# Kernel tuning notes

Hardware: AMD Instinct MI355X
Metric: run time of the kernel (lower is better)

Reference implementation:

```python
import jax, jax.numpy as jnp
import numpy as np

B, L, IN_DIM, H, KD = 2, 2048, 1024, 16, 64
SCALE = float(np.sqrt(IN_DIM / H))  # sqrt(in_dim / num_heads), per ScaledDotAttention
LN_EPS = 1e-5


def setup_inputs() -> dict:
    key = jax.random.key(0)
    ks = jax.random.split(key, 12)
    s_in = 1.0 / np.sqrt(IN_DIM)
    s_hd = 1.0 / np.sqrt(H * KD)
    return {
        "q": jax.random.normal(ks[0], (B, L, IN_DIM), jnp.float32),
        "k": jax.random.normal(ks[1], (B, L, IN_DIM), jnp.float32),
        "v": jax.random.normal(ks[2], (B, L, IN_DIM), jnp.float32),
        "Wq": jax.random.normal(ks[3], (IN_DIM, H * KD), jnp.float32) * s_in,
        "bq": jnp.zeros((H * KD,), jnp.float32),
        "Wk": jax.random.normal(ks[4], (IN_DIM, H * KD), jnp.float32) * s_in,
        "bk": jnp.zeros((H * KD,), jnp.float32),
        "Wv": jax.random.normal(ks[5], (IN_DIM, H * KD), jnp.float32) * s_in,
        "bv": jnp.zeros((H * KD,), jnp.float32),
        "Wo": jax.random.normal(ks[6], (H * KD, IN_DIM), jnp.float32) * s_hd,
        "bo": jnp.zeros((IN_DIM,), jnp.float32),
        "gamma": jnp.ones((IN_DIM,), jnp.float32),
        "beta": jnp.zeros((IN_DIM,), jnp.float32),
    }


def _split_heads(x):
    # [B, L, H*KD] -> [H*B, L, KD]  (heads MAJOR, matching permute(2,0,1,3).view)
    b, l, _ = x.shape
    return x.reshape(b, l, H, KD).transpose(2, 0, 1, 3).reshape(H * b, l, KD)


def reference(q, k, v, Wq, bq, Wk, bk, Wv, bv, Wo, bo, gamma, beta):
    res = q
    qh = _split_heads(q @ Wq + bq)   # [H*B, Lq, KD]
    kh = _split_heads(k @ Wk + bk)
    vh = _split_heads(v @ Wv + bv)
    scores = jnp.einsum("zqd,zkd->zqk", qh, kh) / SCALE
    atn = jax.nn.softmax(scores, axis=-1)          # [H*B, Lq, Lk]
    out = jnp.einsum("zqk,zkd->zqd", atn, vh)      # [H*B, Lq, KD]
    b = q.shape[0]
    out = out.reshape(H, b, -1, KD).transpose(1, 2, 0, 3).reshape(b, -1, H * KD)
    out = out @ Wo + bo
    x = out + res
    mu = jnp.mean(x, axis=-1, keepdims=True)
    var = jnp.mean(jnp.square(x - mu), axis=-1, keepdims=True)
    out = (x - mu) * jax.lax.rsqrt(var + LN_EPS) * gamma + beta
    return (out, atn)
```

## Files before the change

kernel.cpp:

```cpp
#include <hip/hip_runtime.h>
#include <hip/hip_bf16.h>

typedef unsigned short u16;
typedef unsigned int   u32;

using bf16x8 = __attribute__((ext_vector_type(8))) short;
using f32x4  = __attribute__((ext_vector_type(4))) float;

#define SEQ  2048
#define NZ   32
#define KTOT 1024
#define NTOT 1024
#define SC2  0.18033688011112042f

__device__ __forceinline__ u16 f2bf(float f) {
    union { float f; u32 u; } x; x.f = f;
    u32 r = x.u + 0x7fffu + ((x.u >> 16) & 1u);
    return (u16)(r >> 16);
}

__device__ __forceinline__ void gl_lds16(const u16* g, u16* ldsbase) {
    __builtin_amdgcn_global_load_lds(
        (const __attribute__((address_space(1))) u32*)g,
        (__attribute__((address_space(3))) u32*)ldsbase, 16, 0, 0);
}

__global__ __launch_bounds__(256) void prep_k(const float* __restrict__ q,
                                              const float* __restrict__ k,
                                              const float* __restrict__ v,
                                              const float* __restrict__ W0,
                                              const float* __restrict__ W1,
                                              const float* __restrict__ W2,
                                              const float* __restrict__ W3,
                                              u16* __restrict__ qb,
                                              u16* __restrict__ WT) {
    __shared__ u16 t[64 * 65];
    const int tid = threadIdx.x;
    const int b = blockIdx.x;
    if (b < 6144) {
        const int zc = b >> 11;
        const int xc = b & 2047;
        const float* src = (zc == 0) ? q : (zc == 1) ? k : v;
        u16* dst = qb + (size_t)zc * 4096 * 1024;
        int off = xc * 2048 + tid * 8;
        float4 v0 = *(const float4*)&src[off];
        float4 v1 = *(const float4*)&src[off + 4];
        uint4 o;
        o.x = (u32)f2bf(v0.x) | ((u32)f2bf(v0.y) << 16);
        o.y = (u32)f2bf(v0.z) | ((u32)f2bf(v0.w) << 16);
        o.z = (u32)f2bf(v1.x) | ((u32)f2bf(v1.y) << 16);
        o.w = (u32)f2bf(v1.z) | ((u32)f2bf(v1.w) << 16);
        *(uint4*)&dst[off] = o;
        return;
    }
    const int tt = b - 6144;
    const int zz = tt >> 8;
    const int bx = tt & 15, by = (tt >> 4) & 15;
    const float* W = (zz == 0) ? W0 : (zz == 1) ? W1 : (zz == 2) ? W2 : W3;
    u16* out = WT + (size_t)zz * 1024 * 1024;
    const int n0 = bx * 64, k0 = by * 64;
#pragma unroll
    for (int it = 0; it < 4; ++it) {
        int flat = it * 256 + tid;
        int r = flat >> 4, c4 = (flat & 15) * 4;
        float4 vv = *(const float4*)&W[(k0 + r) * 1024 + n0 + c4];
        t[r * 65 + c4 + 0] = f2bf(vv.x);
        t[r * 65 + c4 + 1] = f2bf(vv.y);
        t[r * 65 + c4 + 2] = f2bf(vv.z);
        t[r * 65 + c4 + 3] = f2bf(vv.w);
    }
    __syncthreads();
#pragma unroll
    for (int it = 0; it < 2; ++it) {
        int flat = it * 256 + tid;
        int rn = flat >> 3, c8 = (flat & 7) * 8;
        u32 p[4];
#pragma unroll
        for (int e = 0; e < 4; ++e) {
            u32 lo = t[(c8 + 2 * e + 0) * 65 + rn];
            u32 hi = t[(c8 + 2 * e + 1) * 65 + rn];
            p[e] = lo | (hi << 16);
        }
        uint4 o; o.x = p[0]; o.y = p[1]; o.z = p[2]; o.w = p[3];
        *(uint4*)&out[(n0 + rn) * 1024 + k0 + c8] = o;
    }
}

__global__ __launch_bounds__(256) void qkvproj_k(const u16* __restrict__ qb,
                                                 const u16* __restrict__ wt,
                                                 const float* __restrict__ bq,
                                                 const float* __restrict__ bk,
                                                 const float* __restrict__ bv,
                                                 u16* __restrict__ qh,
                                                 u16* __restrict__ kh,
                                                 u16* __restrict__ vhT) {
    __shared__ u16 As[128 * 32];
    __shared__ u16 Bs[128 * 32];
    __shared__ u16 T[128 * 132];
    const int flat = (blockIdx.z * 32 + blockIdx.y) * 8 + blockIdx.x;
    const int nf   = (flat & 7) * 96 + (flat >> 3);
    const int zz   = nf >> 8;
    const int rem  = nf & 255;
    const int m0   = (rem >> 3) * 128;
    const int n0   = (rem & 7) * 128;

    const u16*   A    = qb + (size_t)zz * 4096 * 1024;
    const u16*   WT   = wt + (size_t)zz * 1024 * 1024;
    const float* bias = (zz == 0) ? bq : (zz == 1) ? bk : bv;
    const bool vmode = (zz == 2);

    const int tid = threadIdx.x;
    const int wid = tid >> 6, lane = tid & 63;
    const int wrow = wid >> 1, wcol = wid & 1;
    const int g = lane >> 4, li = lane & 15;

    f32x4 acc[4][4];
#pragma unroll
    for (int a = 0; a < 4; ++a)
#pragma unroll
        for (int b = 0; b < 4; ++b) acc[a][b] = (f32x4){0.f, 0.f, 0.f, 0.f};

    for (int kt = 0; kt < KTOT / 32; ++kt) {
        const int kb = kt * 32;
#pragma unroll
        for (int cc = 0; cc < 2; ++cc) {
            int c = wid + cc * 4;
            gl_lds16(&A[(m0 + c * 16 + (lane >> 2)) * KTOT + kb + (lane & 3) * 8],
                     &As[c * 512]);
            gl_lds16(&WT[(n0 + c * 16 + (lane >> 2)) * KTOT + kb + (lane & 3) * 8],
                     &Bs[c * 512]);
        }
        __syncthreads();
        bf16x8 af[4], bfr[4];
#pragma unroll
        for (int fr = 0; fr < 4; ++fr)
            af[fr] = *(const bf16x8*)&As[(wrow * 64 + fr * 16 + li) * 32 + g * 8];
#pragma unroll
        for (int fc = 0; fc < 4; ++fc)
            bfr[fc] = *(const bf16x8*)&Bs[(wcol * 64 + fc * 16 + li) * 32 + g * 8];
#pragma unroll
        for (int fr = 0; fr < 4; ++fr)
#pragma unroll
            for (int fc = 0; fc < 4; ++fc)
                acc[fr][fc] = __builtin_amdgcn_mfma_f32_16x16x32_bf16(
                    af[fr], bfr[fc], acc[fr][fc], 0, 0, 0);
        __syncthreads();
    }

#pragma unroll
    for (int fr = 0; fr < 4; ++fr)
#pragma unroll
        for (int fc = 0; fc < 4; ++fc)
#pragma unroll
            for (int reg = 0; reg < 4; ++reg) {
                int rl = wrow * 64 + fr * 16 + g * 4 + reg;
                int cl = wcol * 64 + fc * 16 + li;
                u16 bv16 = f2bf(acc[fr][fc][reg] + bias[n0 + cl]);
                if (!vmode) T[rl * 132 + cl] = bv16;
                else        T[cl * 132 + rl] = bv16;
            }
    __syncthreads();

    const int bb2 = m0 >> 11, ml = m0 & 2047;
    const int lc8 = (tid & 7) * 8;
#pragma unroll
    for (int it = 0; it < 8; ++it) {
        int idx = it * 32 + (tid >> 3);
        int row = idx >> 1, half = idx & 1;
        uint4 val = *(const uint4*)&T[row * 132 + half * 64 + lc8];
        if (!vmode) {
            int h = (n0 >> 6) + half;
            u16* dst = (zz == 0) ? qh : kh;
            *(uint4*)&dst[(((h * 2 + bb2) * 2048 + ml + row) << 6) + lc8] = val;
        } else {
            int cg = n0 + row;
            int h = cg >> 6, d = cg & 63;
            *(uint4*)&vhT[(((h * 2 + bb2) * 64 + d) << 11) + ml + half * 64 + lc8] = val;
        }
    }
}

__global__ __launch_bounds__(256) void outproj_k(const u16* __restrict__ A,
                                                 const u16* __restrict__ WT,
                                                 const float* __restrict__ bias,
                                                 const float* __restrict__ res,
                                                 float* __restrict__ outp) {
    __shared__ u16 As[64 * 32];
    __shared__ u16 Bs[128 * 32];
    const int flat = blockIdx.y * 8 + blockIdx.x;
    const int nf   = (flat & 7) * 64 + (flat >> 3);
    const int m0   = (nf >> 3) * 64;
    const int n0   = (nf & 7) * 128;
    const int tid = threadIdx.x;
    const int wid = tid >> 6, lane = tid & 63;
    const int wrow = wid >> 1, wcol = wid & 1;
    const int g = lane >> 4, li = lane & 15;

    f32x4 acc[2][4];
#pragma unroll
    for (int a = 0; a < 2; ++a)
#pragma unroll
        for (int b = 0; b < 4; ++b) acc[a][b] = (f32x4){0.f, 0.f, 0.f, 0.f};

    for (int kt = 0; kt < KTOT / 32; ++kt) {
        const int kb = kt * 32;
        gl_lds16(&A[(m0 + wid * 16 + (lane >> 2)) * KTOT + kb + (lane & 3) * 8],
                 &As[wid * 512]);
#pragma unroll
        for (int cc = 0; cc < 2; ++cc) {
            int c = wid * 2 + cc;
            gl_lds16(&WT[(n0 + c * 16 + (lane >> 2)) * KTOT + kb + (lane & 3) * 8],
                     &Bs[c * 512]);
        }
        __syncthreads();
        bf16x8 af[2], bfr[4];
#pragma unroll
        for (int fr = 0; fr < 2; ++fr)
            af[fr] = *(const bf16x8*)&As[(wrow * 32 + fr * 16 + li) * 32 + g * 8];
#pragma unroll
        for (int fc = 0; fc < 4; ++fc)
            bfr[fc] = *(const bf16x8*)&Bs[(wcol * 64 + fc * 16 + li) * 32 + g * 8];
#pragma unroll
        for (int fr = 0; fr < 2; ++fr)
#pragma unroll
            for (int fc = 0; fc < 4; ++fc)
                acc[fr][fc] = __builtin_amdgcn_mfma_f32_16x16x32_bf16(
                    af[fr], bfr[fc], acc[fr][fc], 0, 0, 0);
        __syncthreads();
    }

#pragma unroll
    for (int fr = 0; fr < 2; ++fr)
#pragma unroll
        for (int fc = 0; fc < 4; ++fc)
#pragma unroll
            for (int reg = 0; reg < 4; ++reg) {
                int r = m0 + wrow * 32 + fr * 16 + g * 4 + reg;
                int c = n0 + wcol * 64 + fc * 16 + li;
                outp[r * NTOT + c] = acc[fr][fc][reg] + bias[c] + res[r * NTOT + c];
            }
}

__global__ __launch_bounds__(256, 4) void attn_k(const u16* __restrict__ qh,
                                                 const u16* __restrict__ kh,
                                                 const u16* __restrict__ vhT,
                                                 float* __restrict__ atn,
                                                 u16* __restrict__ attnout) {
    __shared__ u16 lds[20480];
    const int tid = threadIdx.x;
    const int D = blockIdx.x;
    const int z = D & 31, q0 = (D >> 5) * 64;
    const int h = z >> 1, bb = z & 1;
    const int wid = tid >> 6, lane = tid & 63, g = lane >> 4, li = lane & 15;
    const int row0 = wid * 16;
    const int zbase = z * SEQ;
    const int swz = li & 7;

    bf16x8 aq[2];
#pragma unroll
    for (int ks = 0; ks < 2; ++ks)
        aq[ks] = *(const bf16x8*)
            &qh[(size_t)(zbase + q0 + row0 + li) * 64 + ks * 32 + g * 8];

    float lmv;
    {
        u16* KsA = lds;
        const int ar = lane >> 3;
        const int ac = (lane & 7) ^ ar;
        const u16* kA[4];
#pragma unroll
        for (int cc = 0; cc < 4; ++cc) {
            int c = wid * 4 + cc;
            kA[cc] = &kh[(size_t)(zbase + c * 8 + ar) * 64 + ac * 8];
            gl_lds16(kA[cc], &KsA[c * 512]);
        }
        __syncthreads();

        float s = 0.f;
        for (int kt = 0; kt < 16; ++kt) {
            const int buf = kt & 1;
            if (kt < 15) {
                const size_t nxt = (size_t)(kt + 1) * 128 * 64;
#pragma unroll
                for (int cc = 0; cc < 4; ++cc)
                    gl_lds16(kA[cc] + nxt,
                             &KsA[(buf ^ 1) * 8192 + (wid * 4 + cc) * 512]);
            }
            f32x4 sv[8];
#pragma unroll
            for (int fc = 0; fc < 8; ++fc) sv[fc] = (f32x4){0.f, 0.f, 0.f, 0.f};
            __builtin_amdgcn_s_setprio(1);
#pragma unroll
            for (int ks = 0; ks < 2; ++ks) {
#pragma unroll
                for (int fc = 0; fc < 8; ++fc) {
                    bf16x8 kf = *(const bf16x8*)
                        &KsA[buf * 8192 + (fc * 16 + li) * 64 + (((ks * 4 + g) ^ swz) * 8)];
                    sv[fc] = __builtin_amdgcn_mfma_f32_16x16x32_bf16(
                        kf, aq[ks], sv[fc], 0, 0, 0);
                }
            }
            __builtin_amdgcn_s_setprio(0);
            float ssum = 0.f;
#pragma unroll
            for (int fc = 0; fc < 8; ++fc)
#pragma unroll
                for (int reg = 0; reg < 4; ++reg)
                    ssum += __builtin_amdgcn_exp2f(sv[fc][reg] * SC2);
            s += ssum;
            __syncthreads();
        }
        s += __shfl_xor(s, 16, 64);
        s += __shfl_xor(s, 32, 64);
        lmv = __builtin_amdgcn_logf(s);
    }

    u16* Ks = lds;
    u16* Vs = lds + 8192;
    u16* Ps = lds + 16384;
    const int ar8 = lane >> 3;
    const int schunk = (lane & 7) ^ ar8;
    const u16* ksrc[2];
    const u16* vsrc[2];
#pragma unroll
    for (int cc = 0; cc < 2; ++cc) {
        int c = wid * 2 + cc;
        ksrc[cc] = &kh[(size_t)(zbase + c * 8 + ar8) * 64 + schunk * 8];
        vsrc[cc] = &vhT[(size_t)(z * 64 + c * 8 + ar8) * SEQ + schunk * 8];
        gl_lds16(ksrc[cc], &Ks[c * 512]);
        gl_lds16(vsrc[cc], &Vs[c * 512]);
    }
    __syncthreads();

    f32x4 oa[4];
#pragma unroll
    for (int fn = 0; fn < 4; ++fn) oa[fn] = (f32x4){0.f, 0.f, 0.f, 0.f};

    const u16* psw = &Ps[wid * 1024];
    const int prow = wid * 1024 + li * 64;
    for (int kt = 0; kt < 32; ++kt) {
        const int buf = kt & 1;
        const int k0 = kt * 64;
        if (kt < 31) {
#pragma unroll
            for (int cc = 0; cc < 2; ++cc) {
                int c = wid * 2 + cc;
                gl_lds16(ksrc[cc] + (size_t)(kt + 1) * 64 * 64,
                         &Ks[(buf ^ 1) * 4096 + c * 512]);
                gl_lds16(vsrc[cc] + (size_t)(kt + 1) * 64,
                         &Vs[(buf ^ 1) * 4096 + c * 512]);
            }
        }

        f32x4 sv[4];
#pragma unroll
        for (int fc = 0; fc < 4; ++fc) sv[fc] = (f32x4){0.f, 0.f, 0.f, 0.f};
        __builtin_amdgcn_s_setprio(1);
#pragma unroll
        for (int ks = 0; ks < 2; ++ks) {
#pragma unroll
            for (int fc = 0; fc < 4; ++fc) {
                bf16x8 kf = *(const bf16x8*)
                    &Ks[buf * 4096 + (fc * 16 + li) * 64 + (((ks * 4 + g) ^ swz) * 8)];
                sv[fc] = __builtin_amdgcn_mfma_f32_16x16x32_bf16(
                    kf, aq[ks], sv[fc], 0, 0, 0);
            }
        }
        __builtin_amdgcn_s_setprio(0);

#pragma unroll
        for (int fc = 0; fc < 4; ++fc) {
            float p0 = __builtin_amdgcn_exp2f(sv[fc][0] * SC2 - lmv);
            float p1 = __builtin_amdgcn_exp2f(sv[fc][1] * SC2 - lmv);
            float p2 = __builtin_amdgcn_exp2f(sv[fc][2] * SC2 - lmv);
            float p3 = __builtin_amdgcn_exp2f(sv[fc][3] * SC2 - lmv);
            uint2 wv2;
            wv2.x = (u32)f2bf(p0) | ((u32)f2bf(p1) << 16);
            wv2.y = (u32)f2bf(p2) | ((u32)f2bf(p3) << 16);
            int pc = ((fc * 2 + (g >> 1)) ^ swz) * 8 + (g & 1) * 4;
            *(uint2*)&Ps[prow + pc] = wv2;
        }

#pragma unroll
        for (int it2 = 0; it2 < 4; ++it2) {
            int row  = it2 * 4 + (lane >> 4);
            int col8 = lane & 15;
            int lc   = col8 >> 1;
            uint2 d2 = *(const uint2*)
                &psw[row * 64 + ((lc ^ (row & 7)) << 3) + ((col8 & 1) << 2)];
            f32x4 o4;
            union { u32 u; float f; } c0v, c1v, c2v, c3v;
            c0v.u = (d2.x & 0xffffu) << 16;  c1v.u = d2.x & 0xffff0000u;
            c2v.u = (d2.y & 0xffffu) << 16;  c3v.u = d2.y & 0xffff0000u;
            o4[0] = c0v.f; o4[1] = c1v.f; o4[2] = c2v.f; o4[3] = c3v.f;
            __builtin_nontemporal_store(o4, (f32x4*)
                &atn[(size_t)(zbase + q0 + row0 + row) * SEQ + k0 + col8 * 4]);
        }

        __builtin_amdgcn_s_setprio(1);
#pragma unroll
        for (int ks = 0; ks < 2; ++ks) {
            bf16x8 pf = *(const bf16x8*)&Ps[prow + (((ks * 4 + g) ^ swz) * 8)];
#pragma unroll
            for (int fn = 0; fn < 4; ++fn) {
                bf16x8 vf = *(const bf16x8*)
                    &Vs[buf * 4096 + (fn * 16 + li) * 64 + (((ks * 4 + g) ^ swz) * 8)];
                oa[fn] = __builtin_amdgcn_mfma_f32_16x16x32_bf16(
                    vf, pf, oa[fn], 0, 0, 0);
            }
        }
        __builtin_amdgcn_s_setprio(0);
        asm volatile("s_waitcnt vmcnt(4) lgkmcnt(0)" ::: "memory");
        __builtin_amdgcn_s_barrier();
    }

#pragma unroll
    for (int fn = 0; fn < 4; ++fn) {
        u32 w0 = (u32)f2bf(oa[fn][0]) | ((u32)f2bf(oa[fn][1]) << 16);
        u32 w1 = (u32)f2bf(oa[fn][2]) | ((u32)f2bf(oa[fn][3]) << 16);
        uint2 wv; wv.x = w0; wv.y = w1;
        *(uint2*)&attnout[(size_t)(bb * SEQ + q0 + row0 + li) * 1024
                          + h * 64 + fn * 16 + g * 4] = wv;
    }
}

__global__ __launch_bounds__(256) void ln_k(const float* __restrict__ y,
                                            const float* __restrict__ gamma,
                                            const float* __restrict__ beta,
                                            float* __restrict__ out) {
    __shared__ float red[8];
    const int row = blockIdx.x, tid = threadIdx.x;
    float4 v = *(const float4*)&y[row * 1024 + tid * 4];
    float s = v.x + v.y + v.z + v.w;
    float sq = v.x * v.x + v.y * v.y + v.z * v.z + v.w * v.w;
#pragma unroll
    for (int msk = 1; msk <= 32; msk <<= 1) {
        s += __shfl_xor(s, msk, 64);
        sq += __shfl_xor(sq, msk, 64);
    }
    const int wid = tid >> 6;
    if ((tid & 63) == 0) { red[wid * 2] = s; red[wid * 2 + 1] = sq; }
    __syncthreads();
    s = red[0] + red[2] + red[4] + red[6];
    sq = red[1] + red[3] + red[5] + red[7];
    float mu = s * (1.0f / 1024.0f);
    float var = sq * (1.0f / 1024.0f) - mu * mu;
    float rs = rsqrtf(var + 1e-5f);
    float4 g4 = *(const float4*)&gamma[tid * 4];
    float4 b4 = *(const float4*)&beta[tid * 4];
    float4 o;
    o.x = (v.x - mu) * rs * g4.x + b4.x;
    o.y = (v.y - mu) * rs * g4.y + b4.y;
    o.z = (v.z - mu) * rs * g4.z + b4.z;
    o.w = (v.w - mu) * rs * g4.w + b4.w;
    *(float4*)&out[row * 1024 + tid * 4] = o;
}

extern "C" void kernel_launch(void* const* d_in, const int* in_sizes, int n_in,
                              void* d_out, int out_size, void* d_ws, size_t ws_size,
                              hipStream_t stream) {
    const float* q     = (const float*)d_in[0];
    const float* k     = (const float*)d_in[1];
    const float* v     = (const float*)d_in[2];
    const float* Wq    = (const float*)d_in[3];
    const float* bq    = (const float*)d_in[4];
    const float* Wk    = (const float*)d_in[5];
    const float* bk    = (const float*)d_in[6];
    const float* Wv    = (const float*)d_in[7];
    const float* bv    = (const float*)d_in[8];
    const float* Wo    = (const float*)d_in[9];
    const float* bo    = (const float*)d_in[10];
    const float* gamma = (const float*)d_in[11];
    const float* beta  = (const float*)d_in[12];

    float* out = (float*)d_out;
    float* atn = out + 4096 * 1024;

    u16* wt  = (u16*)d_ws;
    u16* qb  = wt + 4 * 1024 * 1024;
    u16* attnout = qb;
    float* y = (float*)(qb + 4096 * 1024);
    u16* qh  = qb + 3 * 4096 * 1024;
    u16* kh  = qh + NZ * SEQ * 64;
    u16* vhT = kh + NZ * SEQ * 64;
    u16* wto = wt + 3 * 1024 * 1024;

    dim3 tb(256);
    prep_k<<<dim3(7168), tb, 0, stream>>>(q, k, v, Wq, Wk, Wv, Wo, qb, wt);

    qkvproj_k<<<dim3(8, 32, 3), tb, 0, stream>>>(qb, wt, bq, bk, bv,
                                                 qh, kh, vhT);

    attn_k<<<dim3(1024), tb, 0, stream>>>(qh, kh, vhT, atn, attnout);

    outproj_k<<<dim3(8, 64), tb, 0, stream>>>(attnout, wto, bo, q, y);

    ln_k<<<dim3(4096), tb, 0, stream>>>(y, gamma, beta, out);
}
```

Baseline: 241.6 us.

## Deepen K prefetch pipeline in softmax-denominator pass to 4 buffers

The first attention pass, which computes the softmax log-sum, now streams K in 64-row tiles through a 4-slot LDS ring with loads issued two tiles ahead, instead of 128-row double buffering. The full __syncthreads is replaced by explicit vmcnt/lgkmcnt waits plus s_barrier. This lets global-to-LDS loads overlap more with the MFMA and exp work. In exchange there are twice as many iterations and barriers, and correctness depends on the hand-written waitcnt counts.

Result: slower. 255.3 us (+5.7%).

```diff
diff --git a/kernel.cpp b/kernel.cpp
--- a/kernel.cpp
+++ b/kernel.cpp
@@ -262,53 +262,63 @@
         aq[ks] = *(const bf16x8*)
             &qh[(size_t)(zbase + q0 + row0 + li) * 64 + ks * 32 + g * 8];
 
+    const int ar8 = lane >> 3;
+    const int schunk = (lane & 7) ^ ar8;
+
     float lmv;
     {
         u16* KsA = lds;
-        const int ar = lane >> 3;
-        const int ac = (lane & 7) ^ ar;
-        const u16* kA[4];
-#pragma unroll
-        for (int cc = 0; cc < 4; ++cc) {
-            int c = wid * 4 + cc;
-            kA[cc] = &kh[(size_t)(zbase + c * 8 + ar) * 64 + ac * 8];
-            gl_lds16(kA[cc], &KsA[c * 512]);
-        }
-        __syncthreads();
+        const u16* ksrcA[2];
+#pragma unroll
+        for (int cc = 0; cc < 2; ++cc) {
+            int c = wid * 2 + cc;
+            ksrcA[cc] = &kh[(size_t)(zbase + c * 8 + ar8) * 64 + schunk * 8];
+        }
+#pragma unroll
+        for (int tt = 0; tt < 2; ++tt)
+#pragma unroll
+            for (int cc = 0; cc < 2; ++cc)
+                gl_lds16(ksrcA[cc] + (size_t)tt * 64 * 64,
+                         &KsA[tt * 4096 + (wid * 2 + cc) * 512]);
+        asm volatile("s_waitcnt vmcnt(2) lgkmcnt(0)" ::: "memory");
+        __builtin_amdgcn_s_barrier();
 
         float s = 0.f;
-        for (int kt = 0; kt < 16; ++kt) {
-            const int buf = kt & 1;
-            if (kt < 15) {
-                const size_t nxt = (size_t)(kt + 1) * 128 * 64;
-#pragma unroll
-                for (int cc = 0; cc < 4; ++cc)
-                    gl_lds16(kA[cc] + nxt,
-                             &KsA[(buf ^ 1) * 8192 + (wid * 4 + cc) * 512]);
-            }
-            f32x4 sv[8];
-#pragma unroll
-            for (int fc = 0; fc < 8; ++fc) sv[fc] = (f32x4){0.f, 0.f, 0.f, 0.f};
+        for (int t = 0; t < 32; ++t) {
+            const int buf = t & 3;
+            if (t < 30) {
+#pragma unroll
+                for (int cc = 0; cc < 2; ++cc)
+                    gl_lds16(ksrcA[cc] + (size_t)(t + 2) * 64 * 64,
+                             &KsA[((t + 2) & 3) * 4096 + (wid * 2 + cc) * 512]);
+            }
+            f32x4 sv[4];
+#pragma unroll
+            for (int fc = 0; fc < 4; ++fc) sv[fc] = (f32x4){0.f, 0.f, 0.f, 0.f};
             __builtin_amdgcn_s_setprio(1);
 #pragma unroll
             for (int ks = 0; ks < 2; ++ks) {
 #pragma unroll
-                for (int fc = 0; fc < 8; ++fc) {
+                for (int fc = 0; fc < 4; ++fc) {
                     bf16x8 kf = *(const bf16x8*)
-                        &KsA[buf * 8192 + (fc * 16 + li) * 64 + (((ks * 4 + g) ^ swz) * 8)];
+                        &KsA[buf * 4096 + (fc * 16 + li) * 64 + (((ks * 4 + g) ^ swz) * 8)];
                     sv[fc] = __builtin_amdgcn_mfma_f32_16x16x32_bf16(
                         kf, aq[ks], sv[fc], 0, 0, 0);
                 }
             }
             __builtin_amdgcn_s_setprio(0);
-            float ssum = 0.f;
-#pragma unroll
-            for (int fc = 0; fc < 8; ++fc)
+            float a = 0.f;
+#pragma unroll
+            for (int fc = 0; fc < 4; ++fc)
 #pragma unroll
                 for (int reg = 0; reg < 4; ++reg)
-                    ssum += __builtin_amdgcn_exp2f(sv[fc][reg] * SC2);
-            s += ssum;
-            __syncthreads();
+                    a += __builtin_amdgcn_exp2f(sv[fc][reg] * SC2);
+            s += a;
+            if (t < 30)
+                asm volatile("s_waitcnt vmcnt(2) lgkmcnt(0)" ::: "memory");
+            else
+                asm volatile("s_waitcnt vmcnt(0) lgkmcnt(0)" ::: "memory");
+            __builtin_amdgcn_s_barrier();
         }
         s += __shfl_xor(s, 16, 64);
         s += __shfl_xor(s, 32, 64);
@@ -318,8 +328,6 @@
     u16* Ks = lds;
     u16* Vs = lds + 8192;
     u16* Ps = lds + 16384;
-    const int ar8 = lane >> 3;
-    const int schunk = (lane & 7) ^ ar8;
     const u16* ksrc[2];
     const u16* vsrc[2];
 #pragma unroll
```
